# Kernel optimization log

Hardware: AMD Instinct MI355X
Metric: run time of the kernel (lower is better)

The kernel has to match this reference:

```python
import jax, jax.numpy as jnp
import numpy as np

B, N, C = 8, 1024, 768
H, D = 12, 64  # num_heads, head_dim; C == H*D
SCALE = 1.0 / np.sqrt(D)
NEG_INF = -1e9


def setup_inputs() -> dict:
    key = jax.random.key(0)
    k1, k2, k3, k4 = jax.random.split(key, 4)
    x = jax.random.normal(k1, (B, N, C), dtype=jnp.float32)
    # additive padding mask: 0 for valid tokens, -1e9 for padded tail
    lengths = jax.random.randint(k2, (B,), N // 2, N + 1)  # valid lengths per sample
    pad = jnp.arange(N)[None, :] >= lengths[:, None]       # [B, N] True = padded
    attn_mask = jnp.where(pad, NEG_INF, 0.0).astype(jnp.float32)[:, None, None, :]  # [B,1,1,N]
    W_qkv = jax.random.normal(k3, (C, 3 * C), dtype=jnp.float32) * (C ** -0.5)
    b_qkv = jnp.zeros((3 * C,), dtype=jnp.float32)
    W_proj = jax.random.normal(k4, (C, C), dtype=jnp.float32) * (C ** -0.5)
    b_proj = jnp.zeros((C,), dtype=jnp.float32)
    return {"x": x, "attn_mask": attn_mask, "W_qkv": W_qkv, "b_qkv": b_qkv,
            "W_proj": W_proj, "b_proj": b_proj}


def reference(x, attn_mask, W_qkv, b_qkv, W_proj, b_proj):
    qkv = (x @ W_qkv + b_qkv).reshape(B, N, 3, H, D)
    qkv = jnp.transpose(qkv, (2, 0, 3, 1, 4))
    q, k, v = qkv[0], qkv[1], qkv[2]
    attn = jnp.einsum('bhnd,bhmd->bhnm', q, k) * SCALE  # [B, H, N, N]
    attn = attn + attn_mask                              # broadcast [B,1,1,N]
    attn = jax.nn.softmax(attn, axis=-1)
    out = jnp.einsum('bhnm,bhmd->bhnd', attn, v)         # [B, H, N, D]
    out = jnp.transpose(out, (0, 2, 1, 3)).reshape(B, N, C)
    return out @ W_proj + b_proj
```

## Files before the change

kernel.cpp:

```cpp
#include <hip/hip_runtime.h>
#include <stdint.h>

#define NB 8
#define NHEAD 12
#define SEQ 1024
#define CDIM 768
#define HDIM 64

#define SCALE_L2E 0.1803368801111244f
#define L2E 1.4426950408889634f

typedef __attribute__((ext_vector_type(8))) short bf16x8;
typedef __attribute__((ext_vector_type(4))) short bf16x4;
typedef __attribute__((ext_vector_type(4))) float f32x4;
typedef __attribute__((ext_vector_type(4))) unsigned short us4;

__device__ __forceinline__ void gload_lds16(const void* g, void* l) {
  __builtin_amdgcn_global_load_lds((const __attribute__((address_space(1))) void*)g,
                                   (__attribute__((address_space(3))) void*)l,
                                   16, 0, 0);
}

__device__ __forceinline__ unsigned short f2bf(float f) {
  __bf16 h = (__bf16)f;
  return __builtin_bit_cast(unsigned short, h);
}

__device__ __forceinline__ f32x4 mfma16(bf16x8 a, bf16x8 b, f32x4 c) {
  return __builtin_amdgcn_mfma_f32_16x16x32_bf16(a, b, c, 0, 0, 0);
}


__global__ void cvt_x_kernel(const float* __restrict__ in,
                             unsigned short* __restrict__ out, int n8) {
  int i = blockIdx.x * blockDim.x + threadIdx.x;
  if (i >= n8) return;
  const float4* p = (const float4*)in;
  float4 a = p[2 * i], b = p[2 * i + 1];
  union { bf16x8 v; unsigned short h[8]; } u;
  u.h[0] = f2bf(a.x); u.h[1] = f2bf(a.y); u.h[2] = f2bf(a.z); u.h[3] = f2bf(a.w);
  u.h[4] = f2bf(b.x); u.h[5] = f2bf(b.y); u.h[6] = f2bf(b.z); u.h[7] = f2bf(b.w);
  ((bf16x8*)out)[i] = u.v;
}

__global__ void tconv_kernel(const float* __restrict__ in,
                             unsigned short* __restrict__ out, int K, int N) {
  __shared__ float tile[32][33];
  int tx = threadIdx.x & 31, ty = threadIdx.x >> 5;
  int n0 = blockIdx.x * 32, k0 = blockIdx.y * 32;
#pragma unroll
  for (int i = 0; i < 4; i++)
    tile[ty + 8 * i][tx] = in[(size_t)(k0 + ty + 8 * i) * N + n0 + tx];
  __syncthreads();
#pragma unroll
  for (int i = 0; i < 4; i++)
    out[(size_t)(n0 + ty + 8 * i) * K + k0 + tx] = f2bf(tile[tx][ty + 8 * i]);
}

template <int EPI>
__global__ __launch_bounds__(256, 4)
void gemm_bt_kernel(const unsigned short* __restrict__ A,
                    const unsigned short* __restrict__ Bt,
                    const float* __restrict__ bias,
                    unsigned short* __restrict__ q_out,
                    unsigned short* __restrict__ k_out,
                    unsigned short* __restrict__ v_out,
                    float* __restrict__ f_out,
                    int M, int N, int K) {
  __shared__ __align__(16) unsigned short As[128 * 32];
  __shared__ __align__(16) unsigned short Bs[128 * 32];
  const int t = threadIdx.x;
  const int w = t >> 6, l = t & 63;
  const int g = l >> 4, lr = l & 15;
  const int wr = w >> 1, wc = w & 1;
  const int nTN = N >> 7;
  const int bm = blockIdx.x / nTN, bn = blockIdx.x % nTN;
  const int m0 = bm << 7, n0 = bn << 7;

  f32x4 acc[4][4];
#pragma unroll
  for (int i = 0; i < 4; i++)
#pragma unroll
    for (int j = 0; j < 4; j++) acc[i][j] = f32x4{0.f, 0.f, 0.f, 0.f};

  const int r0c = t >> 2, s0c = t & 3;
  const int r1c = (t + 256) >> 2;
  const int ks0 = s0c ^ ((r0c >> 1) & 3);
  const int ks1 = s0c ^ ((r1c >> 1) & 3);
  const unsigned short* a0 = A + (size_t)(m0 + r0c) * K + ks0 * 8;
  const unsigned short* a1 = A + (size_t)(m0 + r1c) * K + ks1 * 8;
  const unsigned short* b0 = Bt + (size_t)(n0 + r0c) * K + ks0 * 8;
  const unsigned short* b1 = Bt + (size_t)(n0 + r1c) * K + ks1 * 8;
  unsigned short* lA0 = As + t * 8;
  unsigned short* lA1 = As + (t + 256) * 8;
  unsigned short* lB0 = Bs + t * 8;
  unsigned short* lB1 = Bs + (t + 256) * 8;

  const int swr = (lr >> 1) & 3;

  for (int kk = 0; kk < K; kk += 32) {
    gload_lds16(a0 + kk, lA0);
    gload_lds16(a1 + kk, lA1);
    gload_lds16(b0 + kk, lB0);
    gload_lds16(b1 + kk, lB1);
    __syncthreads();
    bf16x8 af[4];
#pragma unroll
    for (int i = 0; i < 4; i++) {
      int row = wr * 64 + i * 16 + lr;
      af[i] = *(const bf16x8*)(As + row * 32 + ((g ^ swr) << 3));
    }
#pragma unroll
    for (int j = 0; j < 4; j++) {
      int row = wc * 64 + j * 16 + lr;
      bf16x8 bfr = *(const bf16x8*)(Bs + row * 32 + ((g ^ swr) << 3));
#pragma unroll
      for (int i = 0; i < 4; i++) acc[i][j] = mfma16(af[i], bfr, acc[i][j]);
    }
    __syncthreads();
  }

  float bv[4];
#pragma unroll
  for (int j = 0; j < 4; j++) bv[j] = bias[n0 + wc * 64 + j * 16 + lr];

  if (EPI == 1) {
#pragma unroll
    for (int i = 0; i < 4; i++) {
      int mrow = m0 + wr * 64 + i * 16 + 4 * g;
#pragma unroll
      for (int j = 0; j < 4; j++) {
        int n = n0 + wc * 64 + j * 16 + lr;
#pragma unroll
        for (int r = 0; r < 4; r++)
          f_out[(size_t)(mrow + r) * N + n] = acc[i][j][r] + bv[j];
      }
    }
  } else {
    const int which = n0 / CDIM;
    const int bb = m0 / SEQ;
    const int tok0 = (m0 % SEQ) + wr * 64;
#pragma unroll
    for (int j = 0; j < 4; j++) {
      int ncol = (n0 % CDIM) + wc * 64 + j * 16;
      int hh = ncol / 64;
      int d = (ncol % 64) + lr;
#pragma unroll
      for (int i = 0; i < 4; i++) {
        int tokb = tok0 + i * 16 + 4 * g;
        if (which == 2) {
          us4 pk;
#pragma unroll
          for (int r = 0; r < 4; r++) pk[r] = f2bf(acc[i][j][r] + bv[j]);
          *(us4*)(v_out + ((size_t)(bb * NHEAD + hh) * 64 + d) * SEQ + tokb) = pk;
        } else {
          unsigned short* dst = (which == 0) ? q_out : k_out;
#pragma unroll
          for (int r = 0; r < 4; r++)
            dst[((size_t)(bb * NHEAD + hh) * SEQ + tokb + r) * 64 + d] =
                f2bf(acc[i][j][r] + bv[j]);
        }
      }
    }
  }
}

__global__ __launch_bounds__(256, 3)
void attn_kernel(const unsigned short* __restrict__ Qb,
                 const unsigned short* __restrict__ Kb,
                 const unsigned short* __restrict__ Vt,
                 const float* __restrict__ mask,
                 unsigned short* __restrict__ Ob) {
  __shared__ __align__(16) unsigned short Qs[128 * 64];
  __shared__ __align__(16) unsigned short Ks[128 * 64];
  __shared__ __align__(16) unsigned short Vs[64 * 128];
  __shared__ __align__(16) float smask[128];

  const int hwb = blockIdx.x;
  const int x = hwb & 7;
  const int i = hwb >> 3;
  const int qt = i & 7;
  const int bh = (i >> 3) * 8 + x;
  const int h = bh % NHEAD, b = bh / NHEAD;

  const int t = threadIdx.x, w = t >> 6, l = t & 63;
  const int g = l >> 4, lr = l & 15;

  const unsigned short* Qg = Qb + (((size_t)b * NHEAD + h) * SEQ + qt * 128) * 64;
  const unsigned short* Kg = Kb + ((size_t)b * NHEAD + h) * SEQ * 64;
  const unsigned short* Vg = Vt + ((size_t)b * NHEAD + h) * 64 * SEQ;
  const float* mg = mask + (size_t)b * SEQ;

  int nkb = 8;
#pragma unroll
  for (int kb = 7; kb >= 4; kb--)
    if (mg[kb * 128] < -1e8f) nkb = kb;

  bf16x8 kreg[4], vreg[4];
  float mreg;
  auto prefetch = [&](int kb) {
#pragma unroll
    for (int ii = 0; ii < 4; ii++) {
      int c = t + 256 * ii;
      int rk = c >> 3, sk = c & 7;
      kreg[ii] = *(const bf16x8*)(Kg + (size_t)(kb * 128 + rk) * 64 +
                                  ((sk ^ (rk & 7)) << 3));
      int rv = c >> 4, sv = c & 15;
      vreg[ii] = *(const bf16x8*)(Vg + (size_t)rv * SEQ + kb * 128 +
                                  ((sv ^ (rv & 7)) << 3));
    }
    mreg = (t < 128) ? mg[kb * 128 + t] * L2E : 0.f;
  };
  auto commit = [&]() {
#pragma unroll
    for (int ii = 0; ii < 4; ii++) {
      *(bf16x8*)(Ks + (t + 256 * ii) * 8) = kreg[ii];
      *(bf16x8*)(Vs + (t + 256 * ii) * 8) = vreg[ii];
    }
    if (t < 128) smask[t] = mreg;
  };

#pragma unroll
  for (int ii = 0; ii < 4; ii++) {
    int c = t + 256 * ii;
    int row = c >> 3, sl = c & 7;
    gload_lds16(Qg + row * 64 + ((sl ^ (row & 7)) << 3), Qs + c * 8);
  }
  prefetch(0);
  __syncthreads();

  bf16x8 qfr[2][2];
#pragma unroll
  for (int qi = 0; qi < 2; qi++)
#pragma unroll
    for (int ks = 0; ks < 2; ks++) {
      int row = w * 32 + qi * 16 + lr;
      qfr[qi][ks] =
          *(const bf16x8*)(Qs + row * 64 + (((ks * 4 + g) ^ (lr & 7)) << 3));
    }

  float l_run[2] = {0.f, 0.f};
  f32x4 oacc[2][4];
#pragma unroll
  for (int qi = 0; qi < 2; qi++)
#pragma unroll
    for (int df = 0; df < 4; df++) oacc[qi][df] = f32x4{0.f, 0.f, 0.f, 0.f};

  for (int kb = 0; kb < nkb; kb++) {
    __syncthreads();
    commit();
    __syncthreads();
    if (kb + 1 < nkb) prefetch(kb + 1);

    float bs[2] = {0.f, 0.f};
    bf16x8 pa[4][2];
#pragma unroll
    for (int kc = 0; kc < 4; kc++) {
      f32x4 s0[2], s1[2];
#pragma unroll
      for (int qi = 0; qi < 2; qi++) {
        s0[qi] = f32x4{0.f, 0.f, 0.f, 0.f};
        s1[qi] = f32x4{0.f, 0.f, 0.f, 0.f};
      }
#pragma unroll
      for (int ks = 0; ks < 2; ks++) {
        int row0 = (2 * kc) * 16 + lr;
        int row1 = (2 * kc + 1) * 16 + lr;
        int slot = ((ks * 4 + g) ^ (lr & 7)) << 3;
        bf16x8 a0 = *(const bf16x8*)(Ks + row0 * 64 + slot);
        bf16x8 a1 = *(const bf16x8*)(Ks + row1 * 64 + slot);
        s0[0] = mfma16(a0, qfr[0][ks], s0[0]);
        s0[1] = mfma16(a0, qfr[1][ks], s0[1]);
        s1[0] = mfma16(a1, qfr[0][ks], s1[0]);
        s1[1] = mfma16(a1, qfr[1][ks], s1[1]);
      }
      f32x4 mv0 = *(const f32x4*)(smask + (2 * kc) * 16 + 4 * g);
      f32x4 mv1 = *(const f32x4*)(smask + (2 * kc + 1) * 16 + 4 * g);
#pragma unroll
      for (int qi = 0; qi < 2; qi++) {
        union { bf16x8 v; unsigned short hh[8]; } u;
#pragma unroll
        for (int r = 0; r < 4; r++) {
          float p0 = __builtin_amdgcn_exp2f(fmaf(s0[qi][r], SCALE_L2E, mv0[r]));
          float p1 = __builtin_amdgcn_exp2f(fmaf(s1[qi][r], SCALE_L2E, mv1[r]));
          bs[qi] += p0 + p1;
          u.hh[r] = f2bf(p0);
          u.hh[4 + r] = f2bf(p1);
        }
        pa[kc][qi] = u.v;
      }
    }
    bs[0] += __shfl_xor(bs[0], 16);
    bs[0] += __shfl_xor(bs[0], 32);
    bs[1] += __shfl_xor(bs[1], 16);
    bs[1] += __shfl_xor(bs[1], 32);
    l_run[0] += bs[0];
    l_run[1] += bs[1];

    const int sw = (lr & 7) << 4;
#pragma unroll
    for (int kc = 0; kc < 4; kc++) {
#pragma unroll
      for (int df = 0; df < 4; df++) {
        const char* vp = (const char*)(Vs + (df * 16 + lr) * 128);
        bf16x4 lo = *(const bf16x4*)(vp + ((kc * 64 + 8 * g) ^ sw));
        bf16x4 hi = *(const bf16x4*)(vp + ((kc * 64 + 32 + 8 * g) ^ sw));
        bf16x8 vb = __builtin_shufflevector(lo, hi, 0, 1, 2, 3, 4, 5, 6, 7);
        oacc[0][df] = mfma16(pa[kc][0], vb, oacc[0][df]);
        oacc[1][df] = mfma16(pa[kc][1], vb, oacc[1][df]);
      }
    }
  }

#pragma unroll
  for (int qi = 0; qi < 2; qi++) {
    float linv = 1.f / l_run[qi];
#pragma unroll
    for (int r = 0; r < 4; r++) {
      float li = __shfl(linv, 4 * g + r);
      int tok = qt * 128 + w * 32 + qi * 16 + 4 * g + r;
#pragma unroll
      for (int df = 0; df < 4; df++) {
        float val = oacc[qi][df][r] * li;
        Ob[((size_t)b * SEQ + tok) * CDIM + h * 64 + df * 16 + lr] = f2bf(val);
      }
    }
  }
}

extern "C" void kernel_launch(void* const* d_in, const int* in_sizes, int n_in,
                              void* d_out, int out_size, void* d_ws,
                              size_t ws_size, hipStream_t stream) {
  const float* x = (const float*)d_in[0];
  const float* mask = (const float*)d_in[1];
  const float* Wqkv = (const float*)d_in[2];
  const float* bqkv = (const float*)d_in[3];
  const float* Wproj = (const float*)d_in[4];
  const float* bproj = (const float*)d_in[5];
  float* out = (float*)d_out;

  char* ws = (char*)d_ws;
  size_t off = 0;
  auto take = [&](size_t bytes) {
    char* p = ws + off;
    off += (bytes + 255) & ~(size_t)255;
    return p;
  };
  unsigned short* xb = (unsigned short*)take((size_t)NB * SEQ * CDIM * 2);
  unsigned short* wqt = (unsigned short*)take((size_t)3 * CDIM * CDIM * 2);
  unsigned short* wpt = (unsigned short*)take((size_t)CDIM * CDIM * 2);
  unsigned short* Qb = (unsigned short*)take((size_t)NB * NHEAD * SEQ * 64 * 2);
  unsigned short* Kbf = (unsigned short*)take((size_t)NB * NHEAD * SEQ * 64 * 2);
  unsigned short* Vt = (unsigned short*)take((size_t)NB * NHEAD * SEQ * 64 * 2);
  unsigned short* Ob = (unsigned short*)take((size_t)NB * SEQ * CDIM * 2);

  int n8 = NB * SEQ * CDIM / 8;
  cvt_x_kernel<<<(n8 + 255) / 256, 256, 0, stream>>>(x, xb, n8);
  tconv_kernel<<<dim3(3 * CDIM / 32, CDIM / 32), 256, 0, stream>>>(Wqkv, wqt,
                                                                   CDIM, 3 * CDIM);
  tconv_kernel<<<dim3(CDIM / 32, CDIM / 32), 256, 0, stream>>>(Wproj, wpt, CDIM,
                                                               CDIM);
  gemm_bt_kernel<0><<<(NB * SEQ / 128) * (3 * CDIM / 128), 256, 0, stream>>>(
      xb, wqt, bqkv, Qb, Kbf, Vt, nullptr, NB * SEQ, 3 * CDIM, CDIM);
  attn_kernel<<<NB * NHEAD * 8, 256, 0, stream>>>(Qb, Kbf, Vt, mask, Ob);
  gemm_bt_kernel<1><<<(NB * SEQ / 128) * (CDIM / 128), 256, 0, stream>>>(
      Ob, wpt, bproj, nullptr, nullptr, nullptr, out, NB * SEQ, CDIM, CDIM);
}
```

Baseline: 212.0 us.

## Double GEMM K-tile to 64 with new XOR swizzle and XCD-aware block remap

The GEMM kernel now stages a 128x64 K-slice per iteration instead of 128x32. This halves the number of barrier pairs per output tile and issues more loads per sync, with a matching 8-way XOR swizzle for LDS bank conflicts. Block indices are also remapped so consecutive tiles land on the same XCD (gridDim/8 stride), aiming for better L2 reuse. LDS usage doubles to 32KB per block, which may lower occupancy under the launch bounds of 4 blocks. The remap assumes the grid size is divisible by 8.

After: 199.0 us. 1.07x faster.

```diff
diff --git a/kernel.cpp b/kernel.cpp
--- a/kernel.cpp
+++ b/kernel.cpp
@@ -67,14 +67,16 @@
                     unsigned short* __restrict__ v_out,
                     float* __restrict__ f_out,
                     int M, int N, int K) {
-  __shared__ __align__(16) unsigned short As[128 * 32];
-  __shared__ __align__(16) unsigned short Bs[128 * 32];
+  __shared__ __align__(16) unsigned short As[128 * 64];
+  __shared__ __align__(16) unsigned short Bs[128 * 64];
   const int t = threadIdx.x;
   const int w = t >> 6, l = t & 63;
   const int g = l >> 4, lr = l & 15;
   const int wr = w >> 1, wc = w & 1;
   const int nTN = N >> 7;
-  const int bm = blockIdx.x / nTN, bn = blockIdx.x % nTN;
+  const int bpx = gridDim.x >> 3;
+  const int orig = (blockIdx.x & 7) * bpx + (blockIdx.x >> 3);
+  const int bm = orig / nTN, bn = orig % nTN;
   const int m0 = bm << 7, n0 = bn << 7;
 
   f32x4 acc[4][4];
@@ -83,39 +85,44 @@
 #pragma unroll
     for (int j = 0; j < 4; j++) acc[i][j] = f32x4{0.f, 0.f, 0.f, 0.f};
 
-  const int r0c = t >> 2, s0c = t & 3;
-  const int r1c = (t + 256) >> 2;
-  const int ks0 = s0c ^ ((r0c >> 1) & 3);
-  const int ks1 = s0c ^ ((r1c >> 1) & 3);
-  const unsigned short* a0 = A + (size_t)(m0 + r0c) * K + ks0 * 8;
-  const unsigned short* a1 = A + (size_t)(m0 + r1c) * K + ks1 * 8;
-  const unsigned short* b0 = Bt + (size_t)(n0 + r0c) * K + ks0 * 8;
-  const unsigned short* b1 = Bt + (size_t)(n0 + r1c) * K + ks1 * 8;
-  unsigned short* lA0 = As + t * 8;
-  unsigned short* lA1 = As + (t + 256) * 8;
-  unsigned short* lB0 = Bs + t * 8;
-  unsigned short* lB1 = Bs + (t + 256) * 8;
-
-  const int swr = (lr >> 1) & 3;
-
-  for (int kk = 0; kk < K; kk += 32) {
-    gload_lds16(a0 + kk, lA0);
-    gload_lds16(a1 + kk, lA1);
-    gload_lds16(b0 + kk, lB0);
-    gload_lds16(b1 + kk, lB1);
+  const unsigned short* aP[4];
+  const unsigned short* bP[4];
+  unsigned short* lA[4];
+  unsigned short* lB[4];
+#pragma unroll
+  for (int i = 0; i < 4; i++) {
+    int c = t + 256 * i;
+    int r = c >> 3, s = c & 7;
+    int ko = (s ^ (r & 7)) * 8;
+    aP[i] = A + (size_t)(m0 + r) * K + ko;
+    bP[i] = Bt + (size_t)(n0 + r) * K + ko;
+    lA[i] = As + c * 8;
+    lB[i] = Bs + c * 8;
+  }
+
+  for (int kk = 0; kk < K; kk += 64) {
+#pragma unroll
+    for (int i = 0; i < 4; i++) {
+      gload_lds16(aP[i] + kk, lA[i]);
+      gload_lds16(bP[i] + kk, lB[i]);
+    }
     __syncthreads();
-    bf16x8 af[4];
-#pragma unroll
-    for (int i = 0; i < 4; i++) {
-      int row = wr * 64 + i * 16 + lr;
-      af[i] = *(const bf16x8*)(As + row * 32 + ((g ^ swr) << 3));
-    }
-#pragma unroll
-    for (int j = 0; j < 4; j++) {
-      int row = wc * 64 + j * 16 + lr;
-      bf16x8 bfr = *(const bf16x8*)(Bs + row * 32 + ((g ^ swr) << 3));
-#pragma unroll
-      for (int i = 0; i < 4; i++) acc[i][j] = mfma16(af[i], bfr, acc[i][j]);
+#pragma unroll
+    for (int ks = 0; ks < 2; ks++) {
+      const int slot = ((ks * 4 + g) ^ (lr & 7)) << 3;
+      bf16x8 af[4];
+#pragma unroll
+      for (int i = 0; i < 4; i++) {
+        int row = wr * 64 + i * 16 + lr;
+        af[i] = *(const bf16x8*)(As + row * 64 + slot);
+      }
+#pragma unroll
+      for (int j = 0; j < 4; j++) {
+        int row = wc * 64 + j * 16 + lr;
+        bf16x8 bfr = *(const bf16x8*)(Bs + row * 64 + slot);
+#pragma unroll
+        for (int i = 0; i < 4; i++) acc[i][j] = mfma16(af[i], bfr, acc[i][j]);
+      }
     }
     __syncthreads();
   }
```
